# Kernel tuning notes

Hardware: AMD Instinct MI355X
Metric: run time of the kernel (lower is better)

## Reference

```python
import jax, jax.numpy as jnp
import numpy as np

D_MODEL = 1024
NUM_EXPERTS = 8
HIDDEN = 2048
TOP_K = 2
SHARED_HIDDEN = 2048
BATCH, SEQ = 4, 2048


def setup_inputs() -> dict:
    key = jax.random.key(0)
    ks = jax.random.split(key, 8)
    s = 1.0 / np.sqrt(D_MODEL)
    sh = 1.0 / np.sqrt(HIDDEN)
    return {
        "x": jax.random.normal(ks[0], (BATCH, SEQ, D_MODEL), dtype=jnp.float32),
        "w_router": jax.random.normal(ks[1], (D_MODEL, NUM_EXPERTS), dtype=jnp.float32) * s,
        "w1": jax.random.normal(ks[2], (NUM_EXPERTS, D_MODEL, HIDDEN), dtype=jnp.float32) * s,
        "w3": jax.random.normal(ks[3], (NUM_EXPERTS, D_MODEL, HIDDEN), dtype=jnp.float32) * s,
        "w2": jax.random.normal(ks[4], (NUM_EXPERTS, HIDDEN, D_MODEL), dtype=jnp.float32) * sh,
        "ws1": jax.random.normal(ks[5], (D_MODEL, SHARED_HIDDEN), dtype=jnp.float32) * s,
        "ws3": jax.random.normal(ks[6], (D_MODEL, SHARED_HIDDEN), dtype=jnp.float32) * s,
        "ws2": jax.random.normal(ks[7], (SHARED_HIDDEN, D_MODEL), dtype=jnp.float32) * sh,
    }


def reference(x, w_router, w1, w3, w2, ws1, ws3, ws2):
    orig_shape = x.shape
    xf = x.reshape(-1, D_MODEL)                       # [T, d]
    T = xf.shape[0]

    # ---- Router: logits -> softmax scores -> top-k weights/indices ----
    logits = xf @ w_router                            # [T, E]
    scores = jax.nn.softmax(logits, axis=-1)          # [T, E]
    expert_weights, expert_indices = jax.lax.top_k(scores, TOP_K)  # [T, K]

    # Dense combine weights: cw[t, e] = routing weight of token t for expert e
    cw = jnp.zeros((T, NUM_EXPERTS), dtype=xf.dtype)
    cw = cw.at[jnp.arange(T)[:, None], expert_indices].add(expert_weights)

    # ---- Experts: per-expert SwiGLU MLP (dense reference for grouped GEMM) ----
    h = jax.nn.silu(jnp.einsum("td,edh->teh", xf, w1)) * jnp.einsum("td,edh->teh", xf, w3)
    y = jnp.einsum("teh,ehd->ted", h, w2)             # [T, E, d]
    moe_out = jnp.einsum("te,ted->td", cw, y)         # [T, d]

    # ---- Shared SwiGLU MLP ----
    shared = (jax.nn.silu(xf @ ws1) * (xf @ ws3)) @ ws2  # [T, d]

    # out = shared/(k+1) + moe * k/(k+1)
    out = shared / (TOP_K + 1) + moe_out * (TOP_K / (TOP_K + 1))
    return out.reshape(orig_shape)
```

## Files before the change

kernel.cpp:

```cpp
#include <hip/hip_runtime.h>
#include <hip/hip_bf16.h>

#define T_TOK 8192
#define DM    1024
#define NE    8
#define HID   2048
#define NP    4096
#define REXP  16384
#define RTOT  24576

typedef __attribute__((ext_vector_type(8))) short bf16x8;
typedef __attribute__((ext_vector_type(4))) float f32x4;

__device__ __forceinline__ unsigned short f2bf(float f) {
  unsigned int u = __float_as_uint(f);
  unsigned int r = (u + 0x7FFFu + ((u >> 16) & 1u)) >> 16;
  return (unsigned short)r;
}

__device__ __forceinline__ void gl2l(const unsigned short* g, unsigned short* l) {
  __builtin_amdgcn_global_load_lds(
      (const __attribute__((address_space(1))) unsigned int*)g,
      (__attribute__((address_space(3))) unsigned int*)l, 16, 0, 0);
}

__global__ void cast_x_k(const float* __restrict__ x, unsigned short* __restrict__ xb) {
  int i = blockIdx.x * 256 + threadIdx.x;
  float4 v = ((const float4*)x)[i];
  ushort4 o;
  o.x = f2bf(v.x); o.y = f2bf(v.y); o.z = f2bf(v.z); o.w = f2bf(v.w);
  ((ushort4*)xb)[i] = o;
}

__global__ void transpose_cast_k(const float* __restrict__ src, unsigned short* __restrict__ dst,
                                 int R, int C) {
  __shared__ float tile[32][33];
  const float* s = src + (size_t)blockIdx.z * R * C;
  unsigned short* d = dst + (size_t)blockIdx.z * R * C;
  int c0 = blockIdx.x * 32, r0 = blockIdx.y * 32;
  int tx = threadIdx.x, ty = threadIdx.y;
#pragma unroll
  for (int i = 0; i < 32; i += 8)
    tile[ty + i][tx] = s[(size_t)(r0 + ty + i) * C + c0 + tx];
  __syncthreads();
#pragma unroll
  for (int i = 0; i < 32; i += 8)
    d[(size_t)(c0 + ty + i) * R + r0 + tx] = f2bf(tile[tx][ty + i]);
}

__global__ void transpose_ilv_k(const float* __restrict__ s1, const float* __restrict__ s3,
                                unsigned short* __restrict__ dst, int R, int C) {
  __shared__ float t1[32][33], t3[32][33];
  const float* a = s1 + (size_t)blockIdx.z * R * C;
  const float* b = s3 + (size_t)blockIdx.z * R * C;
  unsigned short* d = dst + (size_t)blockIdx.z * 2 * R * C;
  int c0 = blockIdx.x * 32, r0 = blockIdx.y * 32;
  int tx = threadIdx.x, ty = threadIdx.y;
#pragma unroll
  for (int i = 0; i < 32; i += 8) {
    t1[ty + i][tx] = a[(size_t)(r0 + ty + i) * C + c0 + tx];
    t3[ty + i][tx] = b[(size_t)(r0 + ty + i) * C + c0 + tx];
  }
  __syncthreads();
#pragma unroll
  for (int i = 0; i < 32; i += 8) {
    int c = c0 + ty + i;
    int f1 = ((c & ~15) << 1) | (c & 15);
    d[(size_t)f1 * R + r0 + tx] = f2bf(t1[tx][ty + i]);
    d[(size_t)(f1 + 16) * R + r0 + tx] = f2bf(t3[tx][ty + i]);
  }
}

__global__ void router_k(const float* __restrict__ x, const float* __restrict__ wr,
                         int* __restrict__ meta, int* __restrict__ te, float* __restrict__ tw) {
  int t = blockIdx.x * 256 + threadIdx.x;
  const float* xr = x + (size_t)t * DM;
  float acc[NE] = {};
  for (int d = 0; d < DM; d += 4) {
    float4 v = *(const float4*)(xr + d);
#pragma unroll
    for (int e = 0; e < NE; ++e) {
      acc[e] += v.x * wr[(d + 0) * NE + e] + v.y * wr[(d + 1) * NE + e]
              + v.z * wr[(d + 2) * NE + e] + v.w * wr[(d + 3) * NE + e];
    }
  }
  float m = acc[0];
#pragma unroll
  for (int e = 1; e < NE; ++e) m = fmaxf(m, acc[e]);
  float p[NE]; float s = 0.f;
#pragma unroll
  for (int e = 0; e < NE; ++e) { p[e] = __expf(acc[e] - m); s += p[e]; }
  float inv = 1.f / s;
  int i0 = 0;
#pragma unroll
  for (int e = 1; e < NE; ++e) if (p[e] > p[i0]) i0 = e;
  int i1 = (i0 == 0) ? 1 : 0;
#pragma unroll
  for (int e = 0; e < NE; ++e) if (e != i0 && p[e] > p[i1]) i1 = e;
  atomicAdd(&meta[i0], 1);
  atomicAdd(&meta[i1], 1);
  te[t * 2 + 0] = i0; te[t * 2 + 1] = i1;
  tw[t * 2 + 0] = p[i0] * inv; tw[t * 2 + 1] = p[i1] * inv;
}

__global__ void scan_k(int* __restrict__ meta) {
  if (threadIdx.x == 0) {
    int* counts = meta; int* roff = meta + 8; int* cursor = meta + 24; int* rcount = meta + 32;
    int acc = 0;
    for (int e = 0; e < NE; ++e) { roff[e] = acc; cursor[e] = acc; rcount[e] = counts[e]; acc += counts[e]; }
    roff[NE] = REXP;
    rcount[NE] = T_TOK;
  }
}

__global__ void build_k(const int* __restrict__ te, const float* __restrict__ tw,
                        int* __restrict__ meta, int* __restrict__ tok_list, float* __restrict__ srow) {
  int t = blockIdx.x * 256 + threadIdx.x;
  int* cursor = meta + 24;
#pragma unroll
  for (int k = 0; k < 2; ++k) {
    int e = te[t * 2 + k];
    int pos = atomicAdd(&cursor[e], 1);
    tok_list[pos] = t;
    srow[pos] = tw[t * 2 + k] * (2.0f / 3.0f);
  }
  tok_list[REXP + t] = t;
  srow[REXP + t] = 1.0f / 3.0f;
}

__global__ __launch_bounds__(256) void gemm1_k(
    const unsigned short* __restrict__ xb,
    const unsigned short* __restrict__ wt13, const unsigned short* __restrict__ wst13,
    unsigned short* __restrict__ Hg,
    const int* __restrict__ tok_list, const int* __restrict__ meta) {
  const int* roff = meta + 8; const int* rcount = meta + 32;
  int e = blockIdx.z;
  int cnt = rcount[e];
  int m0 = blockIdx.y * 128;
  if (m0 >= cnt) return;
  int rbase = roff[e];
  int n0 = blockIdx.x * 128;

  __shared__ int tok_s[128];
  __shared__ __align__(16) unsigned short la[128 * 32];
  __shared__ __align__(16) unsigned short lb[128 * 32];

  int tid = threadIdx.x;
  if (tid < 128) {
    int r = m0 + tid;
    tok_s[tid] = (r < cnt) ? tok_list[rbase + r] : 0;
  }
  __syncthreads();

  const unsigned short* bsrc = (e < NE) ? (wt13 + (size_t)e * NP * DM) : wst13;

  int row0 = tid >> 2, q0 = (tid & 3) << 3;
  int row1 = row0 + 64;
  const unsigned short* ap0 = xb + (size_t)tok_s[row0] * DM + q0;
  const unsigned short* ap1 = xb + (size_t)tok_s[row1] * DM + q0;
  const unsigned short* bp0 = bsrc + (size_t)(n0 + row0) * DM + q0;
  const unsigned short* bp1 = bsrc + (size_t)(n0 + row1) * DM + q0;

  int wave = tid >> 6, lane = tid & 63;
  int wm = (wave >> 1) << 6, wn = (wave & 1) << 6;
  int lq = lane >> 4, lr = lane & 15;

  f32x4 acc[4][4] = {};

  for (int k0 = 0; k0 < DM; k0 += 32) {
    gl2l(ap0, &la[tid * 8]);
    gl2l(ap1, &la[(256 + tid) * 8]);
    gl2l(bp0, &lb[tid * 8]);
    gl2l(bp1, &lb[(256 + tid) * 8]);
    ap0 += 32; ap1 += 32; bp0 += 32; bp1 += 32;
    __syncthreads();
    bf16x8 af[4], bfv[4];
#pragma unroll
    for (int i = 0; i < 4; ++i) {
      af[i]  = *(const bf16x8*)(&la[(wm + i * 16 + lr) * 32 + lq * 8]);
      bfv[i] = *(const bf16x8*)(&lb[(wn + i * 16 + lr) * 32 + lq * 8]);
    }
#pragma unroll
    for (int i = 0; i < 4; ++i)
#pragma unroll
      for (int j = 0; j < 4; ++j)
        acc[i][j] = __builtin_amdgcn_mfma_f32_16x16x32_bf16(af[i], bfv[j], acc[i][j], 0, 0, 0);
    __syncthreads();
  }

  int hbase = (n0 + wn) >> 1;
#pragma unroll
  for (int i = 0; i < 4; ++i)
#pragma unroll
    for (int jp = 0; jp < 2; ++jp)
#pragma unroll
      for (int r = 0; r < 4; ++r) {
        int lm = wm + i * 16 + lq * 4 + r;
        if (m0 + lm < cnt) {
          float a = acc[i][2 * jp][r];
          float c = acc[i][2 * jp + 1][r];
          float h = (a / (1.f + __expf(-a))) * c;
          Hg[(size_t)(rbase + m0 + lm) * HID + hbase + jp * 16 + lr] = f2bf(h);
        }
      }
}

__global__ __launch_bounds__(256) void gemm2_k(
    const unsigned short* __restrict__ Hg,
    const unsigned short* __restrict__ wt2, const unsigned short* __restrict__ wst2,
    float* __restrict__ out,
    const int* __restrict__ tok_list, const float* __restrict__ srow,
    const int* __restrict__ meta) {
  const int* roff = meta + 8; const int* rcount = meta + 32;
  int e = blockIdx.z;
  int cnt = rcount[e];
  int m0 = blockIdx.y * 128;
  if (m0 >= cnt) return;
  int rbase = roff[e];
  int n0 = blockIdx.x * 128;

  __shared__ int tok_s[128];
  __shared__ float sc_s[128];
  __shared__ __align__(16) unsigned short la[128 * 32];
  __shared__ __align__(16) unsigned short lb[128 * 32];

  int tid = threadIdx.x;
  if (tid < 128) {
    int r = m0 + tid;
    tok_s[tid] = (r < cnt) ? tok_list[rbase + r] : -1;
    sc_s[tid] = (r < cnt) ? srow[rbase + r] : 0.f;
  }
  __syncthreads();

  const unsigned short* b = (e < NE) ? (wt2 + (size_t)e * DM * HID) : wst2;

  int wave = tid >> 6, lane = tid & 63;
  int wm = (wave >> 1) << 6, wn = (wave & 1) << 6;
  int lq = lane >> 4, lr = lane & 15;

  int row0 = tid >> 2, q0 = (tid & 3) << 3;
  int row1 = row0 + 64;
  const unsigned short* ap0 = Hg + (size_t)(rbase + m0 + row0) * HID + q0;
  const unsigned short* ap1 = Hg + (size_t)(rbase + m0 + row1) * HID + q0;
  const unsigned short* bp0 = b + (size_t)(n0 + row0) * HID + q0;
  const unsigned short* bp1 = b + (size_t)(n0 + row1) * HID + q0;

  f32x4 acc[4][4] = {};

  for (int k0 = 0; k0 < HID; k0 += 32) {
    gl2l(ap0, &la[tid * 8]);
    gl2l(ap1, &la[(256 + tid) * 8]);
    gl2l(bp0, &lb[tid * 8]);
    gl2l(bp1, &lb[(256 + tid) * 8]);
    ap0 += 32; ap1 += 32; bp0 += 32; bp1 += 32;
    __syncthreads();
    bf16x8 af[4], bfv[4];
#pragma unroll
    for (int i = 0; i < 4; ++i) {
      af[i]  = *(const bf16x8*)(&la[(wm + i * 16 + lr) * 32 + lq * 8]);
      bfv[i] = *(const bf16x8*)(&lb[(wn + i * 16 + lr) * 32 + lq * 8]);
    }
#pragma unroll
    for (int i = 0; i < 4; ++i)
#pragma unroll
      for (int j = 0; j < 4; ++j)
        acc[i][j] = __builtin_amdgcn_mfma_f32_16x16x32_bf16(af[i], bfv[j], acc[i][j], 0, 0, 0);
    __syncthreads();
  }

#pragma unroll
  for (int i = 0; i < 4; ++i)
#pragma unroll
    for (int j = 0; j < 4; ++j)
#pragma unroll
      for (int r = 0; r < 4; ++r) {
        int lm = wm + i * 16 + lq * 4 + r;
        if (m0 + lm < cnt) {
          int tok = tok_s[lm];
          int ln = wn + j * 16 + lr;
          float v = acc[i][j][r] * sc_s[lm];
          unsafeAtomicAdd(&out[(size_t)tok * DM + n0 + ln], v);
        }
      }
}

extern "C" void kernel_launch(void* const* d_in, const int* in_sizes, int n_in,
                              void* d_out, int out_size, void* d_ws, size_t ws_size,
                              hipStream_t stream) {
  const float* x   = (const float*)d_in[0];
  const float* wr  = (const float*)d_in[1];
  const float* w1  = (const float*)d_in[2];
  const float* w3  = (const float*)d_in[3];
  const float* w2  = (const float*)d_in[4];
  const float* ws1 = (const float*)d_in[5];
  const float* ws3 = (const float*)d_in[6];
  const float* ws2 = (const float*)d_in[7];
  float* out = (float*)d_out;

  char* p = (char*)d_ws;
  auto alloc = [&](size_t bytes) { char* r = p; p += (bytes + 255) & ~(size_t)255; return r; };
  unsigned short* xb    = (unsigned short*)alloc((size_t)T_TOK * DM * 2);
  unsigned short* wt13  = (unsigned short*)alloc((size_t)NE * NP * DM * 2);
  unsigned short* wst13 = (unsigned short*)alloc((size_t)NP * DM * 2);
  unsigned short* wt2   = (unsigned short*)alloc((size_t)NE * DM * HID * 2);
  unsigned short* wst2  = (unsigned short*)alloc((size_t)DM * HID * 2);
  unsigned short* Hg    = (unsigned short*)alloc((size_t)RTOT * HID * 2);
  int*   tok_list = (int*)alloc((size_t)RTOT * 4);
  float* srow     = (float*)alloc((size_t)RTOT * 4);
  int*   te       = (int*)alloc((size_t)T_TOK * 2 * 4);
  float* tw       = (float*)alloc((size_t)T_TOK * 2 * 4);
  int*   meta     = (int*)alloc(256);
  (void)ws_size; (void)in_sizes; (void)n_in;

  hipMemsetAsync(meta, 0, 256, stream);
  hipMemsetAsync(out, 0, (size_t)out_size * sizeof(float), stream);

  cast_x_k<<<(T_TOK * DM / 4) / 256, 256, 0, stream>>>(x, xb);

  dim3 tb(32, 8);
  transpose_ilv_k<<<dim3(HID / 32, DM / 32, NE), tb, 0, stream>>>(w1, w3, wt13, DM, HID);
  transpose_ilv_k<<<dim3(HID / 32, DM / 32, 1), tb, 0, stream>>>(ws1, ws3, wst13, DM, HID);
  transpose_cast_k<<<dim3(DM / 32, HID / 32, NE), tb, 0, stream>>>(w2, wt2, HID, DM);
  transpose_cast_k<<<dim3(DM / 32, HID / 32, 1), tb, 0, stream>>>(ws2, wst2, HID, DM);

  router_k<<<T_TOK / 256, 256, 0, stream>>>(x, wr, meta, te, tw);
  scan_k<<<1, 64, 0, stream>>>(meta);
  build_k<<<T_TOK / 256, 256, 0, stream>>>(te, tw, meta, tok_list, srow);

  gemm1_k<<<dim3(NP / 128, 64, NE + 1), 256, 0, stream>>>(xb, wt13, wst13, Hg, tok_list, meta);
  gemm2_k<<<dim3(DM / 128, 64, NE + 1), 256, 0, stream>>>(Hg, wt2, wst2, out, tok_list, srow, meta);
}
```

Baseline: 937.3 us.

## Vectorize weight transposes and replace atomic scatter with buffered combine

Merges the per-expert and shared weight transpose/cast kernels into two launches that use 64x64 tiles with float4 loads and ushort4 stores. Gemm2 now writes scaled per-row results in bf16 into a buffer that reuses the wt13 workspace, instead of atomically adding into the output. A new combine kernel gathers the three contributions per token using recorded positions. This removes the output memset and the float atomics, at the cost of an extra bf16 write/read pass and bf16 rounding of the partial sums.

```diff
diff --git a/kernel.cpp b/kernel.cpp
--- a/kernel.cpp
+++ b/kernel.cpp
@@ -17,6 +17,9 @@
   unsigned int r = (u + 0x7FFFu + ((u >> 16) & 1u)) >> 16;
   return (unsigned short)r;
 }
+__device__ __forceinline__ float b2f(unsigned short h) {
+  return __uint_as_float((unsigned int)h << 16);
+}
 
 __device__ __forceinline__ void gl2l(const unsigned short* g, unsigned short* l) {
   __builtin_amdgcn_global_load_lds(
@@ -32,42 +35,70 @@
   ((ushort4*)xb)[i] = o;
 }
 
-__global__ void transpose_cast_k(const float* __restrict__ src, unsigned short* __restrict__ dst,
-                                 int R, int C) {
-  __shared__ float tile[32][33];
-  const float* s = src + (size_t)blockIdx.z * R * C;
-  unsigned short* d = dst + (size_t)blockIdx.z * R * C;
-  int c0 = blockIdx.x * 32, r0 = blockIdx.y * 32;
-  int tx = threadIdx.x, ty = threadIdx.y;
-#pragma unroll
-  for (int i = 0; i < 32; i += 8)
-    tile[ty + i][tx] = s[(size_t)(r0 + ty + i) * C + c0 + tx];
+__global__ __launch_bounds__(256) void tilv_k(const float* __restrict__ w1, const float* __restrict__ w3,
+                                              const float* __restrict__ s1, const float* __restrict__ s3,
+                                              unsigned short* __restrict__ wt13,
+                                              unsigned short* __restrict__ wst13) {
+  int e = blockIdx.z;
+  const float* a = (e < NE) ? w1 + (size_t)e * DM * HID : s1;
+  const float* b = (e < NE) ? w3 + (size_t)e * DM * HID : s3;
+  unsigned short* d = (e < NE) ? wt13 + (size_t)e * NP * DM : wst13;
+  int c0 = blockIdx.x * 64, r0 = blockIdx.y * 64;
+  __shared__ float t1[64][65], t3[64][65];
+  int tid = threadIdx.x;
+  int rr = tid >> 4;
+  int cc = (tid & 15) << 2;
+#pragma unroll
+  for (int i = 0; i < 64; i += 16) {
+    float4 v1 = *(const float4*)(a + (size_t)(r0 + rr + i) * HID + c0 + cc);
+    float4 v3 = *(const float4*)(b + (size_t)(r0 + rr + i) * HID + c0 + cc);
+    t1[rr + i][cc] = v1.x; t1[rr + i][cc + 1] = v1.y; t1[rr + i][cc + 2] = v1.z; t1[rr + i][cc + 3] = v1.w;
+    t3[rr + i][cc] = v3.x; t3[rr + i][cc + 1] = v3.y; t3[rr + i][cc + 2] = v3.z; t3[rr + i][cc + 3] = v3.w;
+  }
   __syncthreads();
-#pragma unroll
-  for (int i = 0; i < 32; i += 8)
-    d[(size_t)(c0 + ty + i) * R + r0 + tx] = f2bf(tile[tx][ty + i]);
-}
-
-__global__ void transpose_ilv_k(const float* __restrict__ s1, const float* __restrict__ s3,
-                                unsigned short* __restrict__ dst, int R, int C) {
-  __shared__ float t1[32][33], t3[32][33];
-  const float* a = s1 + (size_t)blockIdx.z * R * C;
-  const float* b = s3 + (size_t)blockIdx.z * R * C;
-  unsigned short* d = dst + (size_t)blockIdx.z * 2 * R * C;
-  int c0 = blockIdx.x * 32, r0 = blockIdx.y * 32;
-  int tx = threadIdx.x, ty = threadIdx.y;
-#pragma unroll
-  for (int i = 0; i < 32; i += 8) {
-    t1[ty + i][tx] = a[(size_t)(r0 + ty + i) * C + c0 + tx];
-    t3[ty + i][tx] = b[(size_t)(r0 + ty + i) * C + c0 + tx];
+  int ft0 = tid >> 4;
+  int rt = (tid & 15) << 2;
+#pragma unroll
+  for (int i = 0; i < 4; ++i) {
+    int ft = ft0 + 16 * i;
+    int c = c0 + ft;
+    int f = ((c & ~15) << 1) | (c & 15);
+    ushort4 o1, o3;
+    o1.x = f2bf(t1[rt + 0][ft]); o1.y = f2bf(t1[rt + 1][ft]);
+    o1.z = f2bf(t1[rt + 2][ft]); o1.w = f2bf(t1[rt + 3][ft]);
+    o3.x = f2bf(t3[rt + 0][ft]); o3.y = f2bf(t3[rt + 1][ft]);
+    o3.z = f2bf(t3[rt + 2][ft]); o3.w = f2bf(t3[rt + 3][ft]);
+    *(ushort4*)(d + (size_t)f * DM + r0 + rt) = o1;
+    *(ushort4*)(d + (size_t)(f + 16) * DM + r0 + rt) = o3;
+  }
+}
+
+__global__ __launch_bounds__(256) void w2t_k(const float* __restrict__ w2, const float* __restrict__ s2,
+                                             unsigned short* __restrict__ wt2,
+                                             unsigned short* __restrict__ wst2) {
+  int e = blockIdx.z;
+  const float* a = (e < NE) ? w2 + (size_t)e * HID * DM : s2;
+  unsigned short* d = (e < NE) ? wt2 + (size_t)e * DM * HID : wst2;
+  int c0 = blockIdx.x * 64, r0 = blockIdx.y * 64;
+  __shared__ float t1[64][65];
+  int tid = threadIdx.x;
+  int rr = tid >> 4;
+  int cc = (tid & 15) << 2;
+#pragma unroll
+  for (int i = 0; i < 64; i += 16) {
+    float4 v1 = *(const float4*)(a + (size_t)(r0 + rr + i) * DM + c0 + cc);
+    t1[rr + i][cc] = v1.x; t1[rr + i][cc + 1] = v1.y; t1[rr + i][cc + 2] = v1.z; t1[rr + i][cc + 3] = v1.w;
   }
   __syncthreads();
-#pragma unroll
-  for (int i = 0; i < 32; i += 8) {
-    int c = c0 + ty + i;
-    int f1 = ((c & ~15) << 1) | (c & 15);
-    d[(size_t)f1 * R + r0 + tx] = f2bf(t1[tx][ty + i]);
-    d[(size_t)(f1 + 16) * R + r0 + tx] = f2bf(t3[tx][ty + i]);
+  int ft0 = tid >> 4;
+  int rt = (tid & 15) << 2;
+#pragma unroll
+  for (int i = 0; i < 4; ++i) {
+    int ft = ft0 + 16 * i;
+    ushort4 o;
+    o.x = f2bf(t1[rt + 0][ft]); o.y = f2bf(t1[rt + 1][ft]);
+    o.z = f2bf(t1[rt + 2][ft]); o.w = f2bf(t1[rt + 3][ft]);
+    *(ushort4*)(d + (size_t)(c0 + ft) * HID + r0 + rt) = o;
   }
 }
 
@@ -114,15 +145,17 @@
 }
 
 __global__ void build_k(const int* __restrict__ te, const float* __restrict__ tw,
-                        int* __restrict__ meta, int* __restrict__ tok_list, float* __restrict__ srow) {
+                        int* __restrict__ meta, int* __restrict__ tok_list,
+                        float* __restrict__ srow, int* __restrict__ pos) {
   int t = blockIdx.x * 256 + threadIdx.x;
   int* cursor = meta + 24;
 #pragma unroll
   for (int k = 0; k < 2; ++k) {
     int e = te[t * 2 + k];
-    int pos = atomicAdd(&cursor[e], 1);
-    tok_list[pos] = t;
-    srow[pos] = tw[t * 2 + k] * (2.0f / 3.0f);
+    int q = atomicAdd(&cursor[e], 1);
+    tok_list[q] = t;
+    srow[q] = tw[t * 2 + k] * (2.0f / 3.0f);
+    pos[t * 2 + k] = q;
   }
   tok_list[REXP + t] = t;
   srow[REXP + t] = 1.0f / 3.0f;
@@ -208,9 +241,8 @@
 __global__ __launch_bounds__(256) void gemm2_k(
     const unsigned short* __restrict__ Hg,
     const unsigned short* __restrict__ wt2, const unsigned short* __restrict__ wst2,
-    float* __restrict__ out,
-    const int* __restrict__ tok_list, const float* __restrict__ srow,
-    const int* __restrict__ meta) {
+    unsigned short* __restrict__ yr,
+    const float* __restrict__ srow, const int* __restrict__ meta) {
   const int* roff = meta + 8; const int* rcount = meta + 32;
   int e = blockIdx.z;
   int cnt = rcount[e];
@@ -219,7 +251,6 @@
   int rbase = roff[e];
   int n0 = blockIdx.x * 128;
 
-  __shared__ int tok_s[128];
   __shared__ float sc_s[128];
   __shared__ __align__(16) unsigned short la[128 * 32];
   __shared__ __align__(16) unsigned short lb[128 * 32];
@@ -227,7 +258,6 @@
   int tid = threadIdx.x;
   if (tid < 128) {
     int r = m0 + tid;
-    tok_s[tid] = (r < cnt) ? tok_list[rbase + r] : -1;
     sc_s[tid] = (r < cnt) ? srow[rbase + r] : 0.f;
   }
   __syncthreads();
@@ -276,12 +306,27 @@
       for (int r = 0; r < 4; ++r) {
         int lm = wm + i * 16 + lq * 4 + r;
         if (m0 + lm < cnt) {
-          int tok = tok_s[lm];
           int ln = wn + j * 16 + lr;
-          float v = acc[i][j][r] * sc_s[lm];
-          unsafeAtomicAdd(&out[(size_t)tok * DM + n0 + ln], v);
+          yr[(size_t)(rbase + m0 + lm) * DM + n0 + ln] = f2bf(acc[i][j][r] * sc_s[lm]);
         }
       }
+}
+
+__global__ __launch_bounds__(256) void combine_k(const unsigned short* __restrict__ yr,
+                                                 const int* __restrict__ pos,
+                                                 float* __restrict__ out) {
+  int t = blockIdx.x;
+  int p0 = pos[2 * t], p1 = pos[2 * t + 1];
+  int d = threadIdx.x << 2;
+  ushort4 a = *(const ushort4*)(yr + (size_t)p0 * DM + d);
+  ushort4 b = *(const ushort4*)(yr + (size_t)p1 * DM + d);
+  ushort4 c = *(const ushort4*)(yr + (size_t)(REXP + t) * DM + d);
+  float4 o;
+  o.x = b2f(a.x) + b2f(b.x) + b2f(c.x);
+  o.y = b2f(a.y) + b2f(b.y) + b2f(c.y);
+  o.z = b2f(a.z) + b2f(b.z) + b2f(c.z);
+  o.w = b2f(a.w) + b2f(b.w) + b2f(c.w);
+  *(float4*)(out + (size_t)t * DM + d) = o;
 }
 
 extern "C" void kernel_launch(void* const* d_in, const int* in_sizes, int n_in,
@@ -309,24 +354,23 @@
   float* srow     = (float*)alloc((size_t)RTOT * 4);
   int*   te       = (int*)alloc((size_t)T_TOK * 2 * 4);
   float* tw       = (float*)alloc((size_t)T_TOK * 2 * 4);
+  int*   pos      = (int*)alloc((size_t)T_TOK * 2 * 4);
   int*   meta     = (int*)alloc(256);
+  unsigned short* yr = wt13;
   (void)ws_size; (void)in_sizes; (void)n_in;
 
   hipMemsetAsync(meta, 0, 256, stream);
-  hipMemsetAsync(out, 0, (size_t)out_size * sizeof(float), stream);
 
   cast_x_k<<<(T_TOK * DM / 4) / 256, 256, 0, stream>>>(x, xb);
 
-  dim3 tb(32, 8);
-  transpose_ilv_k<<<dim3(HID / 32, DM / 32, NE), tb, 0, stream>>>(w1, w3, wt13, DM, HID);
-  transpose_ilv_k<<<dim3(HID / 32, DM / 32, 1), tb, 0, stream>>>(ws1, ws3, wst13, DM, HID);
-  transpose_cast_k<<<dim3(DM / 32, HID / 32, NE), tb, 0, stream>>>(w2, wt2, HID, DM);
-  transpose_cast_k<<<dim3(DM / 32, HID / 32, 1), tb, 0, stream>>>(ws2, wst2, HID, DM);
+  tilv_k<<<dim3(HID / 64, DM / 64, NE + 1), 256, 0, stream>>>(w1, w3, ws1, ws3, wt13, wst13);
+  w2t_k<<<dim3(DM / 64, HID / 64, NE + 1), 256, 0, stream>>>(w2, ws2, wt2, wst2);
 
   router_k<<<T_TOK / 256, 256, 0, stream>>>(x, wr, meta, te, tw);
   scan_k<<<1, 64, 0, stream>>>(meta);
-  build_k<<<T_TOK / 256, 256, 0, stream>>>(te, tw, meta, tok_list, srow);
+  build_k<<<T_TOK / 256, 256, 0, stream>>>(te, tw, meta, tok_list, srow, pos);
 
   gemm1_k<<<dim3(NP / 128, 64, NE + 1), 256, 0, stream>>>(xb, wt13, wst13, Hg, tok_list, meta);
-  gemm2_k<<<dim3(DM / 128, 64, NE + 1), 256, 0, stream>>>(Hg, wt2, wst2, out, tok_list, srow, meta);
-}
+  gemm2_k<<<dim3(DM / 128, 64, NE + 1), 256, 0, stream>>>(Hg, wt2, wst2, yr, srow, meta);
+  combine_k<<<T_TOK, 256, 0, stream>>>(yr, pos, out);
+}
```

After: 892.9 us. -4.7%, faster.
